# Kernel tuning notes

Hardware: AMD Instinct MI355X
Metric: run time of the kernel (lower is better)

Reference implementation:

```python
import jax, jax.numpy as jnp
import numpy as np

N_NODES = 100_000
N_EDGES = 1_600_000
DIM_IN = 256
ADD_TO_EDGE_SCORE = 0.5  # PyG EdgePooling default


def setup_inputs() -> dict:
    key = jax.random.key(0)
    k1, k2, k3 = jax.random.split(key, 3)
    x = jax.random.normal(k1, (N_NODES, DIM_IN), dtype=jnp.float32)
    edge_index = jax.random.randint(k2, (2, N_EDGES), 0, N_NODES, dtype=jnp.int32)
    batch = jnp.zeros((N_NODES,), dtype=jnp.int32)  # single graph
    W = jax.random.normal(k3, (2 * DIM_IN, 1), dtype=jnp.float32) / np.sqrt(2.0 * DIM_IN)
    b = jnp.zeros((1,), dtype=jnp.float32)
    return {"x": x, "edge_index": edge_index, "batch": batch, "W": W, "b": b}


def _segment_softmax(scores, seg, num_segments):
    m = jax.ops.segment_max(scores, seg, num_segments=num_segments)
    ex = jnp.exp(scores - m[seg])
    s = jax.ops.segment_sum(ex, seg, num_segments=num_segments)
    return ex / s[seg]


def _greedy_matching(rank, src, dst, num_nodes):
    """Maximal matching equivalent to sequential greedy over edges sorted by
    ascending rank (rank = position in descending-score argsort, a strict total
    order). Implemented as parallel locally-dominant matching rounds."""
    big = jnp.iinfo(jnp.int32).max

    def cond(state):
        alive, matched, chosen = state
        return jnp.any(alive)

    def body(state):
        alive, matched, chosen = state
        r = jnp.where(alive, rank, big)
        node_min = jnp.full((num_nodes,), big, dtype=jnp.int32)
        node_min = node_min.at[src].min(r)
        node_min = node_min.at[dst].min(r)
        # an alive edge is picked if it dominates all alive edges at both endpoints
        pick = alive & (rank == node_min[src]) & (rank == node_min[dst])
        matched = matched.at[jnp.where(pick, src, num_nodes)].set(True, mode='drop')
        matched = matched.at[jnp.where(pick, dst, num_nodes)].set(True, mode='drop')
        chosen = chosen | pick
        alive = alive & ~matched[src] & ~matched[dst]
        return alive, matched, chosen

    alive0 = jnp.ones_like(rank, dtype=bool)
    matched0 = jnp.zeros((num_nodes,), dtype=bool)
    chosen0 = jnp.zeros_like(alive0)
    _, matched, chosen = jax.lax.while_loop(cond, body, (alive0, matched0, chosen0))
    return chosen, matched


def reference(x, edge_index, batch, W, b):
    num_nodes, feat = x.shape
    num_edges = edge_index.shape[1]
    src, dst = edge_index[0], edge_index[1]

    # Linear([x_src || x_dst]) split to avoid materializing [E, 2F]
    s_src = x @ W[:feat, 0]   # [N]
    s_dst = x @ W[feat:, 0]   # [N]
    raw = s_src[src] + s_dst[dst] + b[0]            # [E]
    # dropout is identity in eval mode
    e = _segment_softmax(raw, dst, num_nodes) + ADD_TO_EDGE_SCORE  # [E]

    # rank: position of each edge in descending-score order
    order = jnp.argsort(-e)
    rank = jnp.zeros((num_edges,), dtype=jnp.int32).at[order].set(
        jnp.arange(num_edges, dtype=jnp.int32))

    chosen, matched = _greedy_matching(rank, src, dst, num_nodes)

    # cluster id of each chosen edge = its position among chosen edges in score order
    chosen_sorted = chosen[order]
    cid_sorted = jnp.cumsum(chosen_sorted.astype(jnp.int32)) - 1
    cid = jnp.zeros((num_edges,), dtype=jnp.int32).at[order].set(cid_sorted)
    num_matched = jnp.sum(chosen.astype(jnp.int32))

    # node -> cluster assignment; unmatched nodes get trailing singleton clusters
    cluster = jnp.zeros((num_nodes,), dtype=jnp.int32)
    cluster = cluster.at[jnp.where(chosen, src, num_nodes)].set(cid, mode='drop')
    cluster = cluster.at[jnp.where(chosen, dst, num_nodes)].set(cid, mode='drop')
    unm = num_matched + jnp.cumsum((~matched).astype(jnp.int32)) - 1
    cluster = jnp.where(matched, cluster, unm)
    num_clusters = num_matched + jnp.sum((~matched).astype(jnp.int32))

    # per-cluster score: chosen-edge scores for merged pairs, 1.0 for singletons
    new_edge_score = jnp.ones((num_nodes,), dtype=x.dtype)
    new_edge_score = new_edge_score.at[jnp.where(chosen, cid, num_nodes)].set(e, mode='drop')

    # scatter-merge node features (rows >= num_clusters are zero padding)
    new_x = jax.ops.segment_sum(x, cluster, num_segments=num_nodes)
    new_x = new_x * new_edge_score[:, None]

    new_edge_index = cluster[edge_index]  # remapped edges (coalesce/dedup omitted)
    new_batch = jnp.zeros((num_nodes,), dtype=batch.dtype).at[cluster].set(batch)

    return new_x, new_edge_index, new_batch, num_clusters
```

## Files before the change

### kernel.cpp

```cpp
#include <hip/hip_runtime.h>

typedef unsigned int u32;
typedef unsigned long long u64;
typedef unsigned char u8;

static constexpr int SORTN   = 65536;
static constexpr int STILE   = 2048;
static constexpr int NROUNDS = 20;

__device__ __forceinline__ u32 ordf(float f) {
  u32 u = __float_as_uint(f);
  return (u & 0x80000000u) ? ~u : (u | 0x80000000u);
}
__device__ __forceinline__ float inv_ordf(u32 m) {
  return __uint_as_float((m & 0x80000000u) ? (m ^ 0x80000000u) : ~m);
}

__global__ __launch_bounds__(256)
void k_init(u32* m_ord, double* ssum, u8* matched, u64* node_min,
            float* scoreC, ulonglong2* sortbuf, u32* fcnt, u32* scalars,
            int N, int E) {
  int i = blockIdx.x * blockDim.x + threadIdx.x;
  if (i < N) {
    m_ord[i] = 0u; ssum[i] = 0.0; matched[i] = 0;
    node_min[i] = ~0ull; node_min[(size_t)N + i] = ~0ull;
    scoreC[i] = 1.0f;
  }
  if (i < SORTN) sortbuf[i] = make_ulonglong2(~0ull, ~0ull);
  if (i < 256)   fcnt[i] = 0u;
  if (i < 16)    scalars[i] = 0u;
  if (i == 0)    fcnt[0] = (u32)E;
}

__global__ __launch_bounds__(256)
void k_dots(const float4* __restrict__ x4, const float4* __restrict__ W4,
            float* __restrict__ s_src, float* __restrict__ s_dst, int N) {
  int gt = blockIdx.x * blockDim.x + threadIdx.x;
  int w = gt >> 6, lane = gt & 63;
  if (w >= N) return;
  float4 xa = x4[(size_t)w * 64 + lane];
  float4 wa = W4[lane];
  float4 wb = W4[64 + lane];
  float pa = xa.x*wa.x + xa.y*wa.y + xa.z*wa.z + xa.w*wa.w;
  float pb = xa.x*wb.x + xa.y*wb.y + xa.z*wb.z + xa.w*wb.w;
  #pragma unroll
  for (int m = 32; m >= 1; m >>= 1) {
    pa += __shfl_xor(pa, m);
    pb += __shfl_xor(pb, m);
  }
  if (lane == 0) { s_src[w] = pa; s_dst[w] = pb; }
}

__global__ __launch_bounds__(256)
void k_max(const int* __restrict__ src, const int* __restrict__ dst,
           const float* __restrict__ s_src, const float* __restrict__ s_dst,
           const float* __restrict__ bvec, u32* m_ord, int E) {
  int e = blockIdx.x * blockDim.x + threadIdx.x;
  if (e >= E) return;
  int d = dst[e];
  float r = s_src[src[e]] + s_dst[d] + bvec[0];
  atomicMax(&m_ord[d], ordf(r));
}

__global__ __launch_bounds__(256)
void k_expsum(const int* __restrict__ src, const int* __restrict__ dst,
              const float* __restrict__ s_src, const float* __restrict__ s_dst,
              const float* __restrict__ bvec, const u32* __restrict__ m_ord,
              double* ssum, int E) {
  int e = blockIdx.x * blockDim.x + threadIdx.x;
  if (e >= E) return;
  int d = dst[e];
  float r = s_src[src[e]] + s_dst[d] + bvec[0];
  float ex = expf(r - inv_ordf(m_ord[d]));
  atomicAdd(&ssum[d], (double)ex);
}

__global__ __launch_bounds__(256)
void k_scorekey(const int* __restrict__ src, const int* __restrict__ dst,
                const float* __restrict__ s_src, const float* __restrict__ s_dst,
                const float* __restrict__ bvec, const u32* __restrict__ m_ord,
                const double* __restrict__ ssum,
                ulonglong2* __restrict__ front0, int E) {
  int e = blockIdx.x * blockDim.x + threadIdx.x;
  if (e >= E) return;
  int s = src[e], d = dst[e];
  float r = s_src[s] + s_dst[d] + bvec[0];
  float ex = expf(r - inv_ordf(m_ord[d]));
  float es = ex / (float)ssum[d] + 0.5f;
  u64 key = ((u64)(~ordf(es)) << 32) | (u32)e;
  u64 sd  = ((u64)(u32)s << 32) | (u32)d;
  front0[e] = make_ulonglong2(key, sd);
}

template<int R>
__global__ __launch_bounds__(256)
void k_mmin(const ulonglong2* __restrict__ fin, const u32* __restrict__ cntp,
            const u8* __restrict__ matched, u64* nm) {
  u32 cnt = *cntp;
  u32 nth = gridDim.x * 256;
  for (u32 i = blockIdx.x * 256 + threadIdx.x; i < cnt; i += nth) {
    ulonglong2 t = fin[i];
    int s = (int)(t.y >> 32), d = (int)(u32)t.y;
    if (matched[s] | matched[d]) continue;
    atomicMin(&nm[s], t.x);
    if (d != s) atomicMin(&nm[d], t.x);
  }
}

template<int R>
__global__ __launch_bounds__(256)
void k_mpick(const ulonglong2* __restrict__ fin, const u32* __restrict__ cntp,
             const u64* __restrict__ nm, u64* nmNext, u8* matched,
             ulonglong2* fout, u32* cntOut, ulonglong2* sortbuf, u32* scalars) {
  __shared__ u32 wb[4];
  __shared__ u32 bbase;
  u32 cnt = *cntp;
  int tx = threadIdx.x, lane = tx & 63, wid = tx >> 6;
  for (u32 base = blockIdx.x * 256; base < cnt; base += gridDim.x * 256) {
    u32 gid = base + tx;
    ulonglong2 t = make_ulonglong2(0ull, 0ull);
    int s = 0, d = 0;
    bool pk = false, surv = false;
    if (gid < cnt) {
      t = fin[gid];
      s = (int)(t.y >> 32); d = (int)(u32)t.y;
      if (!(matched[s] | matched[d])) {
        if (nm[s] == t.x && nm[d] == t.x) pk = true; else surv = true;
      }
    }
    u64 pm = __ballot(pk);
    if (pm) {
      u32 pre = (u32)__popcll(pm & ((1ull << lane) - 1ull));
      int ldr = __ffsll((long long)pm) - 1;
      u32 pb = 0;
      if (lane == ldr) pb = atomicAdd(&scalars[0], (u32)__popcll(pm));
      pb = __shfl(pb, ldr);
      if (pk) {
        matched[s] = 1; matched[d] = 1;
        sortbuf[pb + pre] = t;
      }
    }
    u64 sm = __ballot(surv);
    if (lane == 0) wb[wid] = (u32)__popcll(sm);
    __syncthreads();
    if (tx == 0) {
      u32 tt = wb[0] + wb[1] + wb[2] + wb[3];
      bbase = tt ? atomicAdd(cntOut, tt) : 0u;
    }
    __syncthreads();
    if (surv) {
      u32 woff = 0;
      for (int w = 0; w < wid; w++) woff += wb[w];
      u32 pre = (u32)__popcll(sm & ((1ull << lane) - 1ull));
      fout[bbase + woff + pre] = t;
      nmNext[s] = ~0ull;
      nmNext[d] = ~0ull;
    }
    __syncthreads();
  }
}

__global__ __launch_bounds__(1024)
void k_mfinish(ulonglong2* fA, ulonglong2* fB, u8* matched, u64* nm,
               ulonglong2* sortbuf, const u32* __restrict__ cntp, u32* scalars) {
  __shared__ u32 sh_cnt;
  u32 cnt = *cntp;
  int tx = threadIdx.x;
  ulonglong2* fin = fA; ulonglong2* fout = fB;
  while (cnt > 0) {
    for (u32 i = tx; i < cnt; i += 1024) {
      u64 p = fin[i].y;
      nm[p >> 32] = ~0ull; nm[(u32)p] = ~0ull;
    }
    if (tx == 0) sh_cnt = 0;
    __syncthreads();
    for (u32 i = tx; i < cnt; i += 1024) {
      ulonglong2 t = fin[i];
      int s = (int)(t.y >> 32), d = (int)(u32)t.y;
      if (matched[s] | matched[d]) continue;
      atomicMin(&nm[s], t.x);
      if (d != s) atomicMin(&nm[d], t.x);
    }
    __syncthreads();
    for (u32 i = tx; i < cnt; i += 1024) {
      ulonglong2 t = fin[i];
      int s = (int)(t.y >> 32), d = (int)(u32)t.y;
      if (matched[s] | matched[d]) continue;
      u64 a = atomicAdd(&nm[s], 0ull);
      u64 b = (d == s) ? a : atomicAdd(&nm[d], 0ull);
      if (a == t.x && b == t.x) {
        matched[s] = 1; matched[d] = 1;
        u32 o = atomicAdd(&scalars[0], 1u);
        sortbuf[o] = t;
      } else {
        u32 o = atomicAdd(&sh_cnt, 1u);
        fout[o] = t;
      }
    }
    __syncthreads();
    cnt = sh_cnt;
    ulonglong2* tmp = fin; fin = fout; fout = tmp;
    __syncthreads();
  }
}

__global__ __launch_bounds__(256)
void k_sort1(ulonglong2* buf) {
  __shared__ ulonglong2 t[STILE];
  const int base = blockIdx.x * STILE;
  for (int i = threadIdx.x; i < STILE; i += 256) t[i] = buf[base + i];
  __syncthreads();
  for (int k = 2; k <= STILE; k <<= 1) {
    for (int j = k >> 1; j > 0; j >>= 1) {
      for (int i = threadIdx.x; i < STILE; i += 256) {
        int p = i ^ j;
        if (p > i) {
          bool dir = (((base + i) & k) == 0);
          ulonglong2 a = t[i], c = t[p];
          if ((a.x > c.x) == dir) { t[i] = c; t[p] = a; }
        }
      }
      __syncthreads();
    }
  }
  for (int i = threadIdx.x; i < STILE; i += 256) buf[base + i] = t[i];
}

__global__ __launch_bounds__(256)
void k_gpass(ulonglong2* buf, int j, int k) {
  int i = blockIdx.x * 256 + threadIdx.x;
  int p = i ^ j;
  if (p > i && p < SORTN) {
    bool dir = ((i & k) == 0);
    ulonglong2 a = buf[i], c = buf[p];
    if ((a.x > c.x) == dir) { buf[i] = c; buf[p] = a; }
  }
}

__global__ __launch_bounds__(256)
void k_sortl(ulonglong2* buf, int k) {
  __shared__ ulonglong2 t[STILE];
  const int base = blockIdx.x * STILE;
  const bool dir = ((base & k) == 0);
  for (int i = threadIdx.x; i < STILE; i += 256) t[i] = buf[base + i];
  __syncthreads();
  for (int j = STILE >> 1; j > 0; j >>= 1) {
    for (int i = threadIdx.x; i < STILE; i += 256) {
      int p = i ^ j;
      if (p > i) {
        ulonglong2 a = t[i], c = t[p];
        if ((a.x > c.x) == dir) { t[i] = c; t[p] = a; }
      }
    }
    __syncthreads();
  }
  for (int i = threadIdx.x; i < STILE; i += 256) buf[base + i] = t[i];
}

__global__ __launch_bounds__(256)
void k_assign(const ulonglong2* __restrict__ buf,
              int* cluster, int* memA, int* memB, float* scoreC,
              const u32* __restrict__ scalars) {
  int i = blockIdx.x * blockDim.x + threadIdx.x;
  if (i >= (int)scalars[0]) return;
  ulonglong2 t = buf[i];
  int s = (int)(t.y >> 32), d = (int)(u32)t.y;
  cluster[s] = i; cluster[d] = i;
  scoreC[i] = inv_ordf(~(u32)(t.x >> 32));
  memA[i] = s;
  memB[i] = (s == d) ? -1 : d;
}

__global__ __launch_bounds__(256)
void k_scan1(const u8* __restrict__ matched, u32* partials, int N) {
  __shared__ u32 sh[256];
  int b = blockIdx.x, tx = threadIdx.x;
  int v0 = b * 1024 + tx * 4;
  u32 c = 0;
  #pragma unroll
  for (int q = 0; q < 4; q++) { int v = v0 + q; if (v < N && !matched[v]) c++; }
  sh[tx] = c; __syncthreads();
  for (int s = 128; s > 0; s >>= 1) { if (tx < s) sh[tx] += sh[tx + s]; __syncthreads(); }
  if (tx == 0) partials[b] = sh[0];
}

__global__ void k_scan2(const u32* partials, u32* partials2, u32* scalars, int NB) {
  if (blockIdx.x == 0 && threadIdx.x == 0) {
    u32 run = 0;
    for (int i = 0; i < NB; i++) { partials2[i] = run; run += partials[i]; }
    scalars[1] = run;
    scalars[2] = scalars[0] + run;
  }
}

__global__ __launch_bounds__(256)
void k_scan3(const u8* __restrict__ matched, const u32* __restrict__ partials2,
             const u32* __restrict__ scalars, int* cluster, int* memA, int* memB, int N) {
  __shared__ u32 sh[256];
  int b = blockIdx.x, tx = threadIdx.x;
  int v0 = b * 1024 + tx * 4;
  u32 f[4]; u32 c = 0;
  #pragma unroll
  for (int q = 0; q < 4; q++) { int v = v0 + q; f[q] = (v < N && !matched[v]); c += f[q]; }
  sh[tx] = c; __syncthreads();
  for (int s = 1; s < 256; s <<= 1) {
    u32 x = sh[tx];
    u32 y = (tx >= s) ? sh[tx - s] : 0;
    __syncthreads();
    sh[tx] = x + y;
    __syncthreads();
  }
  u32 base = scalars[0] + partials2[b] + (sh[tx] - c);
  #pragma unroll
  for (int q = 0; q < 4; q++) {
    if (f[q]) {
      int v = v0 + q;
      int cc = (int)base++;
      cluster[v] = cc; memA[cc] = v; memB[cc] = -1;
    }
  }
}

__global__ __launch_bounds__(256)
void k_newx(const float4* __restrict__ x4, const int* __restrict__ memA,
            const int* __restrict__ memB, const float* __restrict__ scoreC,
            const u32* __restrict__ scalars, float4* __restrict__ out4, int N) {
  int gt = blockIdx.x * blockDim.x + threadIdx.x;
  int w = gt >> 6, lane = gt & 63;
  if (w >= N) return;
  int nc = (int)scalars[2];
  float4 o;
  if (w < nc) {
    int a = memA[w], b = memB[w];
    float s = scoreC[w];
    float4 va = x4[(size_t)a * 64 + lane];
    float ox = va.x, oy = va.y, oz = va.z, ow = va.w;
    if (b >= 0) {
      float4 vb = x4[(size_t)b * 64 + lane];
      ox += vb.x; oy += vb.y; oz += vb.z; ow += vb.w;
    }
    o = make_float4(ox * s, oy * s, oz * s, ow * s);
  } else {
    o = make_float4(0.f, 0.f, 0.f, 0.f);
  }
  out4[(size_t)w * 64 + lane] = o;
}

__global__ __launch_bounds__(256)
void k_remap(const int* __restrict__ ei, const int* __restrict__ cluster,
             float* __restrict__ outE, int twoE) {
  int i = blockIdx.x * blockDim.x + threadIdx.x;
  if (i < twoE) outE[i] = (float)cluster[ei[i]];
}

__global__ __launch_bounds__(256)
void k_tail(float* __restrict__ outB, const u32* __restrict__ scalars, int N) {
  int i = blockIdx.x * blockDim.x + threadIdx.x;
  if (i < N) outB[i] = 0.0f;
  if (i == 0) outB[N] = (float)scalars[2];
}

template<int R>
static void launch_rounds(ulonglong2* frontA, ulonglong2* frontB, u64* node_min,
                          u8* matched, ulonglong2* sortbuf, u32* fcnt, u32* scalars,
                          int N, int NB_E, hipStream_t stream) {
  if constexpr (R < NROUNDS) {
    ulonglong2* fin  = (R & 1) ? frontB : frontA;
    ulonglong2* fout = (R & 1) ? frontA : frontB;
    u64* nm  = node_min + (size_t)(R & 1) * N;
    u64* nmN = node_min + (size_t)((R & 1) ^ 1) * N;
    int nbr = NB_E >> R; if (nbr < 256) nbr = 256;
    k_mmin<R><<<nbr, 256, 0, stream>>>(fin, fcnt + R, matched, nm);
    k_mpick<R><<<nbr, 256, 0, stream>>>(fin, fcnt + R, nm, nmN, matched,
                                        fout, fcnt + R + 1, sortbuf, scalars);
    launch_rounds<R + 1>(frontA, frontB, node_min, matched, sortbuf, fcnt, scalars,
                         N, NB_E, stream);
  }
}

extern "C" void kernel_launch(void* const* d_in, const int* in_sizes, int n_in,
                              void* d_out, int out_size, void* d_ws, size_t ws_size,
                              hipStream_t stream) {
  const float* x    = (const float*)d_in[0];
  const int*   ei   = (const int*)d_in[1];
  const float* W    = (const float*)d_in[3];
  const float* bvec = (const float*)d_in[4];
  int N = in_sizes[2];
  int E = in_sizes[1] / 2;

  char* p = (char*)d_ws;
  auto alloc = [&](size_t bytes) { char* r = p; p += (bytes + 255) & ~(size_t)255; return r; };
  float*      s_src    = (float*)alloc((size_t)N * 4);
  float*      s_dst    = (float*)alloc((size_t)N * 4);
  u32*        m_ord    = (u32*)alloc((size_t)N * 4);
  double*     ssum     = (double*)alloc((size_t)N * 8);
  ulonglong2* frontA   = (ulonglong2*)alloc((size_t)E * 16);
  ulonglong2* frontB   = (ulonglong2*)alloc((size_t)E * 16);
  u8*         matched  = (u8*)alloc((size_t)N);
  u64*        node_min = (u64*)alloc((size_t)2 * N * 8);
  ulonglong2* sortbuf  = (ulonglong2*)alloc((size_t)SORTN * 16);
  int*        cluster  = (int*)alloc((size_t)N * 4);
  int*        memA     = (int*)alloc((size_t)N * 4);
  int*        memB     = (int*)alloc((size_t)N * 4);
  float*      scoreC   = (float*)alloc((size_t)N * 4);
  u32*        fcnt     = (u32*)alloc(1024);
  u32*        partials = (u32*)alloc(4096);
  u32*        partials2= (u32*)alloc(4096);
  u32*        scalars  = (u32*)alloc(256);
  (void)ws_size; (void)out_size; (void)n_in;

  const int* srcp = ei;
  const int* dstp = ei + E;
  float* out  = (float*)d_out;
  float* outX = out;
  float* outE = out + (size_t)N * 256;
  float* outB = outE + (size_t)2 * E;

  int NB_E = (E + 255) / 256;
  int cover = (N > SORTN) ? N : SORTN;
  k_init<<<(cover + 255) / 256, 256, 0, stream>>>(m_ord, ssum, matched, node_min,
                                                  scoreC, sortbuf, fcnt, scalars, N, E);
  k_dots<<<((size_t)N * 64 + 255) / 256, 256, 0, stream>>>(
      (const float4*)x, (const float4*)W, s_src, s_dst, N);
  k_max<<<NB_E, 256, 0, stream>>>(srcp, dstp, s_src, s_dst, bvec, m_ord, E);
  k_expsum<<<NB_E, 256, 0, stream>>>(srcp, dstp, s_src, s_dst, bvec, m_ord, ssum, E);
  k_scorekey<<<NB_E, 256, 0, stream>>>(srcp, dstp, s_src, s_dst, bvec, m_ord, ssum,
                                       frontA, E);

  launch_rounds<0>(frontA, frontB, node_min, matched, sortbuf, fcnt, scalars,
                   N, NB_E, stream);
  k_mfinish<<<1, 1024, 0, stream>>>(frontA, frontB, matched, node_min, sortbuf,
                                    fcnt + NROUNDS, scalars);

  k_sort1<<<SORTN / STILE, 256, 0, stream>>>(sortbuf);
  for (int k = STILE << 1; k <= SORTN; k <<= 1) {
    for (int j = k >> 1; j >= STILE; j >>= 1)
      k_gpass<<<SORTN / 256, 256, 0, stream>>>(sortbuf, j, k);
    k_sortl<<<SORTN / STILE, 256, 0, stream>>>(sortbuf, k);
  }

  k_assign<<<SORTN / 256, 256, 0, stream>>>(sortbuf, cluster, memA, memB, scoreC, scalars);
  int NB = (N + 1023) / 1024;
  k_scan1<<<NB, 256, 0, stream>>>(matched, partials, N);
  k_scan2<<<1, 64, 0, stream>>>(partials, partials2, scalars, NB);
  k_scan3<<<NB, 256, 0, stream>>>(matched, partials2, scalars, cluster, memA, memB, N);

  k_newx<<<((size_t)N * 64 + 255) / 256, 256, 0, stream>>>(
      (const float4*)x, memA, memB, scoreC, scalars, (float4*)outX, N);
  k_remap<<<(2 * E + 255) / 256, 256, 0, stream>>>(ei, cluster, outE, 2 * E);
  k_tail<<<(N + 255) / 256, 256, 0, stream>>>(outB, scalars, N);
}
```

Before: 1.444 ms.

## Privatize scatter atomics per XCD and fuse first matching min into scorekey

The softmax max/sum scatters and the heavy early matching-round node-min scatters now go to per-XCD private copies. The copy is chosen by reading the hardware XCC id, and the atomics use workgroup scope. Small merge kernels then reduce the eight copies. The first round's node-min pass is folded into the score-key kernel. The number of multi-block rounds drops from 20 to 12, so the single-block finisher handles a longer tail. The aim is to cut cross-die atomic traffic on device-scope atomics, at the cost of extra memory, extra merge passes and a correctness reliance on the XCC-id mapping and workgroup-scope semantics.

```diff
diff --git a/kernel.cpp b/kernel.cpp
--- a/kernel.cpp
+++ b/kernel.cpp
@@ -4,9 +4,27 @@
 typedef unsigned long long u64;
 typedef unsigned char u8;
 
-static constexpr int SORTN   = 65536;
-static constexpr int STILE   = 2048;
-static constexpr int NROUNDS = 20;
+static constexpr int SORTN = 65536;
+static constexpr int STILE = 2048;
+static constexpr int NR    = 12;
+static constexpr int NHEAVY= 3;
+static constexpr int NXCD  = 8;
+
+__device__ __forceinline__ u32 xccid() {
+  u32 x;
+  asm volatile("s_getreg_b32 %0, hwreg(HW_REG_XCC_ID)" : "=s"(x));
+  return x & (NXCD - 1);
+}
+
+__device__ __forceinline__ void wmin64(u64* p, u64 v) {
+  __hip_atomic_fetch_min(p, v, __ATOMIC_RELAXED, __HIP_MEMORY_SCOPE_WORKGROUP);
+}
+__device__ __forceinline__ void wmax32(u32* p, u32 v) {
+  __hip_atomic_fetch_max(p, v, __ATOMIC_RELAXED, __HIP_MEMORY_SCOPE_WORKGROUP);
+}
+__device__ __forceinline__ void waddf64(double* p, double v) {
+  __hip_atomic_fetch_add(p, v, __ATOMIC_RELAXED, __HIP_MEMORY_SCOPE_WORKGROUP);
+}
 
 __device__ __forceinline__ u32 ordf(float f) {
   u32 u = __float_as_uint(f);
@@ -17,15 +35,13 @@
 }
 
 __global__ __launch_bounds__(256)
-void k_init(u32* m_ord, double* ssum, u8* matched, u64* node_min,
-            float* scoreC, ulonglong2* sortbuf, u32* fcnt, u32* scalars,
-            int N, int E) {
+void k_init(u32* m_ord, u32* m8, double* ssum, double* ss8, u8* matched,
+            u64* node_min, u64* nm8, float* scoreC, ulonglong2* sortbuf,
+            u32* fcnt, u32* scalars, int N, int E) {
   int i = blockIdx.x * blockDim.x + threadIdx.x;
-  if (i < N) {
-    m_ord[i] = 0u; ssum[i] = 0.0; matched[i] = 0;
-    node_min[i] = ~0ull; node_min[(size_t)N + i] = ~0ull;
-    scoreC[i] = 1.0f;
-  }
+  if (i < N) { m_ord[i] = 0u; ssum[i] = 0.0; matched[i] = 0; scoreC[i] = 1.0f; }
+  if (i < 2 * N) node_min[i] = ~0ull;
+  if (i < NXCD * N) { nm8[i] = ~0ull; m8[i] = 0u; ss8[i] = 0.0; }
   if (i < SORTN) sortbuf[i] = make_ulonglong2(~0ull, ~0ull);
   if (i < 256)   fcnt[i] = 0u;
   if (i < 16)    scalars[i] = 0u;
@@ -52,27 +68,52 @@
 }
 
 __global__ __launch_bounds__(256)
-void k_max(const int* __restrict__ src, const int* __restrict__ dst,
-           const float* __restrict__ s_src, const float* __restrict__ s_dst,
-           const float* __restrict__ bvec, u32* m_ord, int E) {
+void k_max8(const int* __restrict__ src, const int* __restrict__ dst,
+            const float* __restrict__ s_src, const float* __restrict__ s_dst,
+            const float* __restrict__ bvec, u32* m8, int N, int E) {
   int e = blockIdx.x * blockDim.x + threadIdx.x;
   if (e >= E) return;
+  u32* mW = m8 + (size_t)xccid() * N;
   int d = dst[e];
   float r = s_src[src[e]] + s_dst[d] + bvec[0];
-  atomicMax(&m_ord[d], ordf(r));
-}
-
-__global__ __launch_bounds__(256)
-void k_expsum(const int* __restrict__ src, const int* __restrict__ dst,
-              const float* __restrict__ s_src, const float* __restrict__ s_dst,
-              const float* __restrict__ bvec, const u32* __restrict__ m_ord,
-              double* ssum, int E) {
+  wmax32(&mW[d], ordf(r));
+}
+
+__global__ __launch_bounds__(256)
+void k_maxmerge(const u32* __restrict__ m8, u32* __restrict__ m_ord, int N) {
+  int v = blockIdx.x * 256 + threadIdx.x;
+  if (v >= N) return;
+  u32 m = 0u;
+  #pragma unroll
+  for (int x = 0; x < NXCD; x++) {
+    u32 t = m8[(size_t)x * N + v];
+    m = (t > m) ? t : m;
+  }
+  m_ord[v] = m;
+}
+
+__global__ __launch_bounds__(256)
+void k_expsum8(const int* __restrict__ src, const int* __restrict__ dst,
+               const float* __restrict__ s_src, const float* __restrict__ s_dst,
+               const float* __restrict__ bvec, const u32* __restrict__ m_ord,
+               double* ss8, int N, int E) {
   int e = blockIdx.x * blockDim.x + threadIdx.x;
   if (e >= E) return;
+  double* sW = ss8 + (size_t)xccid() * N;
   int d = dst[e];
   float r = s_src[src[e]] + s_dst[d] + bvec[0];
   float ex = expf(r - inv_ordf(m_ord[d]));
-  atomicAdd(&ssum[d], (double)ex);
+  waddf64(&sW[d], (double)ex);
+}
+
+__global__ __launch_bounds__(256)
+void k_ssmerge(const double* __restrict__ ss8, double* __restrict__ ssum, int N) {
+  int v = blockIdx.x * 256 + threadIdx.x;
+  if (v >= N) return;
+  double s = 0.0;
+  #pragma unroll
+  for (int x = 0; x < NXCD; x++) s += ss8[(size_t)x * N + v];
+  ssum[v] = s;
 }
 
 __global__ __launch_bounds__(256)
@@ -80,9 +121,10 @@
                 const float* __restrict__ s_src, const float* __restrict__ s_dst,
                 const float* __restrict__ bvec, const u32* __restrict__ m_ord,
                 const double* __restrict__ ssum,
-                ulonglong2* __restrict__ front0, int E) {
+                ulonglong2* __restrict__ front0, u64* nm8, int N, int E) {
   int e = blockIdx.x * blockDim.x + threadIdx.x;
   if (e >= E) return;
+  u64* nmW = nm8 + (size_t)xccid() * N;
   int s = src[e], d = dst[e];
   float r = s_src[s] + s_dst[d] + bvec[0];
   float ex = expf(r - inv_ordf(m_ord[d]));
@@ -90,12 +132,44 @@
   u64 key = ((u64)(~ordf(es)) << 32) | (u32)e;
   u64 sd  = ((u64)(u32)s << 32) | (u32)d;
   front0[e] = make_ulonglong2(key, sd);
+  wmin64(&nmW[s], key);
+  if (d != s) wmin64(&nmW[d], key);
+}
+
+__global__ __launch_bounds__(256)
+void k_merge(u64* nm8, u64* __restrict__ nmOut, int N) {
+  int v = blockIdx.x * 256 + threadIdx.x;
+  if (v >= N) return;
+  u64 m = ~0ull;
+  #pragma unroll
+  for (int x = 0; x < NXCD; x++) {
+    size_t idx = (size_t)x * N + v;
+    u64 t = nm8[idx];
+    if (t != ~0ull) { nm8[idx] = ~0ull; m = (t < m) ? t : m; }
+  }
+  nmOut[v] = m;
 }
 
 template<int R>
 __global__ __launch_bounds__(256)
-void k_mmin(const ulonglong2* __restrict__ fin, const u32* __restrict__ cntp,
-            const u8* __restrict__ matched, u64* nm) {
+void k_mmin_h(const ulonglong2* __restrict__ fin, const u32* __restrict__ cntp,
+              const u8* __restrict__ matched, u64* nm8, int N) {
+  u32 cnt = *cntp;
+  u64* nmW = nm8 + (size_t)xccid() * N;
+  u32 nth = gridDim.x * 256;
+  for (u32 i = blockIdx.x * 256 + threadIdx.x; i < cnt; i += nth) {
+    ulonglong2 t = fin[i];
+    int s = (int)(t.y >> 32), d = (int)(u32)t.y;
+    if (matched[s] | matched[d]) continue;
+    wmin64(&nmW[s], t.x);
+    if (d != s) wmin64(&nmW[d], t.x);
+  }
+}
+
+template<int R>
+__global__ __launch_bounds__(256)
+void k_mmin_l(const ulonglong2* __restrict__ fin, const u32* __restrict__ cntp,
+              const u8* __restrict__ matched, u64* nm) {
   u32 cnt = *cntp;
   u32 nth = gridDim.x * 256;
   for (u32 i = blockIdx.x * 256 + threadIdx.x; i < cnt; i += nth) {
@@ -125,7 +199,8 @@
       t = fin[gid];
       s = (int)(t.y >> 32); d = (int)(u32)t.y;
       if (!(matched[s] | matched[d])) {
-        if (nm[s] == t.x && nm[d] == t.x) pk = true; else surv = true;
+        pk = (nm[s] == t.x) && (nm[d] == t.x);
+        surv = !pk;
       }
     }
     u64 pm = __ballot(pk);
@@ -135,10 +210,7 @@
       u32 pb = 0;
       if (lane == ldr) pb = atomicAdd(&scalars[0], (u32)__popcll(pm));
       pb = __shfl(pb, ldr);
-      if (pk) {
-        matched[s] = 1; matched[d] = 1;
-        sortbuf[pb + pre] = t;
-      }
+      if (pk) { matched[s] = 1; matched[d] = 1; sortbuf[pb + pre] = t; }
     }
     u64 sm = __ballot(surv);
     if (lane == 0) wb[wid] = (u32)__popcll(sm);
@@ -154,7 +226,7 @@
       u32 pre = (u32)__popcll(sm & ((1ull << lane) - 1ull));
       fout[bbase + woff + pre] = t;
       nmNext[s] = ~0ull;
-      nmNext[d] = ~0ull;
+      if (d != s) nmNext[d] = ~0ull;
     }
     __syncthreads();
   }
@@ -178,16 +250,19 @@
       ulonglong2 t = fin[i];
       int s = (int)(t.y >> 32), d = (int)(u32)t.y;
       if (matched[s] | matched[d]) continue;
-      atomicMin(&nm[s], t.x);
-      if (d != s) atomicMin(&nm[d], t.x);
+      wmin64(&nm[s], t.x);
+      if (d != s) wmin64(&nm[d], t.x);
     }
     __syncthreads();
     for (u32 i = tx; i < cnt; i += 1024) {
       ulonglong2 t = fin[i];
       int s = (int)(t.y >> 32), d = (int)(u32)t.y;
       if (matched[s] | matched[d]) continue;
-      u64 a = atomicAdd(&nm[s], 0ull);
-      u64 b = (d == s) ? a : atomicAdd(&nm[d], 0ull);
+      u64 a = __hip_atomic_fetch_add(&nm[s], 0ull, __ATOMIC_RELAXED,
+                                     __HIP_MEMORY_SCOPE_WORKGROUP);
+      u64 b = (d == s) ? a
+            : __hip_atomic_fetch_add(&nm[d], 0ull, __ATOMIC_RELAXED,
+                                     __HIP_MEMORY_SCOPE_WORKGROUP);
       if (a == t.x && b == t.x) {
         matched[s] = 1; matched[d] = 1;
         u32 o = atomicAdd(&scalars[0], 1u);
@@ -361,20 +436,27 @@
 }
 
 template<int R>
-static void launch_rounds(ulonglong2* frontA, ulonglong2* frontB, u64* node_min,
-                          u8* matched, ulonglong2* sortbuf, u32* fcnt, u32* scalars,
-                          int N, int NB_E, hipStream_t stream) {
-  if constexpr (R < NROUNDS) {
+static void launch_rounds(ulonglong2* frontA, ulonglong2* frontB, u64* nm8,
+                          u64* node_min, u8* matched, ulonglong2* sortbuf,
+                          u32* fcnt, u32* scalars, int N, int NB_E,
+                          hipStream_t stream) {
+  if constexpr (R < NR) {
     ulonglong2* fin  = (R & 1) ? frontB : frontA;
     ulonglong2* fout = (R & 1) ? frontA : frontB;
     u64* nm  = node_min + (size_t)(R & 1) * N;
     u64* nmN = node_min + (size_t)((R & 1) ^ 1) * N;
     int nbr = NB_E >> R; if (nbr < 256) nbr = 256;
-    k_mmin<R><<<nbr, 256, 0, stream>>>(fin, fcnt + R, matched, nm);
+    if constexpr (R == 0) {
+    } else if constexpr (R < NHEAVY) {
+      k_mmin_h<R><<<nbr, 256, 0, stream>>>(fin, fcnt + R, matched, nm8, N);
+      k_merge<<<(N + 255) / 256, 256, 0, stream>>>(nm8, nm, N);
+    } else {
+      k_mmin_l<R><<<nbr, 256, 0, stream>>>(fin, fcnt + R, matched, nm);
+    }
     k_mpick<R><<<nbr, 256, 0, stream>>>(fin, fcnt + R, nm, nmN, matched,
                                         fout, fcnt + R + 1, sortbuf, scalars);
-    launch_rounds<R + 1>(frontA, frontB, node_min, matched, sortbuf, fcnt, scalars,
-                         N, NB_E, stream);
+    launch_rounds<R + 1>(frontA, frontB, nm8, node_min, matched, sortbuf,
+                         fcnt, scalars, N, NB_E, stream);
   }
 }
 
@@ -393,11 +475,14 @@
   float*      s_src    = (float*)alloc((size_t)N * 4);
   float*      s_dst    = (float*)alloc((size_t)N * 4);
   u32*        m_ord    = (u32*)alloc((size_t)N * 4);
+  u32*        m8       = (u32*)alloc((size_t)NXCD * N * 4);
   double*     ssum     = (double*)alloc((size_t)N * 8);
+  double*     ss8      = (double*)alloc((size_t)NXCD * N * 8);
   ulonglong2* frontA   = (ulonglong2*)alloc((size_t)E * 16);
   ulonglong2* frontB   = (ulonglong2*)alloc((size_t)E * 16);
   u8*         matched  = (u8*)alloc((size_t)N);
   u64*        node_min = (u64*)alloc((size_t)2 * N * 8);
+  u64*        nm8      = (u64*)alloc((size_t)NXCD * N * 8);
   ulonglong2* sortbuf  = (ulonglong2*)alloc((size_t)SORTN * 16);
   int*        cluster  = (int*)alloc((size_t)N * 4);
   int*        memA     = (int*)alloc((size_t)N * 4);
@@ -417,20 +502,24 @@
   float* outB = outE + (size_t)2 * E;
 
   int NB_E = (E + 255) / 256;
-  int cover = (N > SORTN) ? N : SORTN;
-  k_init<<<(cover + 255) / 256, 256, 0, stream>>>(m_ord, ssum, matched, node_min,
-                                                  scoreC, sortbuf, fcnt, scalars, N, E);
+  int cover = NXCD * N; if (cover < SORTN) cover = SORTN;
+  k_init<<<(cover + 255) / 256, 256, 0, stream>>>(m_ord, m8, ssum, ss8, matched,
+                                                  node_min, nm8, scoreC, sortbuf,
+                                                  fcnt, scalars, N, E);
   k_dots<<<((size_t)N * 64 + 255) / 256, 256, 0, stream>>>(
       (const float4*)x, (const float4*)W, s_src, s_dst, N);
-  k_max<<<NB_E, 256, 0, stream>>>(srcp, dstp, s_src, s_dst, bvec, m_ord, E);
-  k_expsum<<<NB_E, 256, 0, stream>>>(srcp, dstp, s_src, s_dst, bvec, m_ord, ssum, E);
+  k_max8<<<NB_E, 256, 0, stream>>>(srcp, dstp, s_src, s_dst, bvec, m8, N, E);
+  k_maxmerge<<<(N + 255) / 256, 256, 0, stream>>>(m8, m_ord, N);
+  k_expsum8<<<NB_E, 256, 0, stream>>>(srcp, dstp, s_src, s_dst, bvec, m_ord, ss8, N, E);
+  k_ssmerge<<<(N + 255) / 256, 256, 0, stream>>>(ss8, ssum, N);
   k_scorekey<<<NB_E, 256, 0, stream>>>(srcp, dstp, s_src, s_dst, bvec, m_ord, ssum,
-                                       frontA, E);
-
-  launch_rounds<0>(frontA, frontB, node_min, matched, sortbuf, fcnt, scalars,
+                                       frontA, nm8, N, E);
+  k_merge<<<(N + 255) / 256, 256, 0, stream>>>(nm8, node_min, N);
+
+  launch_rounds<0>(frontA, frontB, nm8, node_min, matched, sortbuf, fcnt, scalars,
                    N, NB_E, stream);
-  k_mfinish<<<1, 1024, 0, stream>>>(frontA, frontB, matched, node_min, sortbuf,
-                                    fcnt + NROUNDS, scalars);
+  k_mfinish<<<1, 1024, 0, stream>>>(frontA, frontB, matched, node_min,
+                                    sortbuf, fcnt + NR, scalars);
 
   k_sort1<<<SORTN / STILE, 256, 0, stream>>>(sortbuf);
   for (int k = STILE << 1; k <= SORTN; k <<= 1) {
```

Result: slower. 1.596 ms (+10.5%).
